# Optimization experiments

Measured on AMD Instinct MI355X. Metric: run time of the kernel, lower is better.

## Reference

```python
import jax, jax.numpy as jnp
import numpy as np

B, T, D, H = 4, 1024, 1024, 16
HD = D // H
EPS = 1e-5


def setup_inputs() -> dict:
    key = jax.random.key(0)
    ks = jax.random.split(key, 8)
    input_tensor = jax.random.normal(ks[0], (B, T, D), dtype=jnp.float32)
    # contiguous valid prefixes (realistic padding mask); True = valid
    lengths = jax.random.randint(ks[1], (B,), T // 2, T + 1)
    sequence_mask = jnp.arange(T)[None, :] < lengths[:, None]
    # online attention mask: causal (True = position allowed)
    attn_mask = jnp.tril(jnp.ones((T, T), dtype=bool))
    scale = 1.0 / np.sqrt(D)
    in_proj_w = jax.random.normal(ks[2], (3 * D, D), dtype=jnp.float32) * scale
    in_proj_b = jnp.zeros((3 * D,), dtype=jnp.float32)
    out_w = jax.random.normal(ks[3], (D, D), dtype=jnp.float32) * scale
    out_b = jnp.zeros((D,), dtype=jnp.float32)
    ln_gamma = jnp.ones((D,), dtype=jnp.float32)
    ln_beta = jnp.zeros((D,), dtype=jnp.float32)
    return {
        "input_tensor": input_tensor,
        "ln_gamma": ln_gamma,
        "ln_beta": ln_beta,
        "in_proj_w": in_proj_w,
        "in_proj_b": in_proj_b,
        "out_w": out_w,
        "out_b": out_b,
        "sequence_mask": sequence_mask,
        "attn_mask": attn_mask,
    }


def reference(input_tensor, ln_gamma, ln_beta, in_proj_w, in_proj_b, out_w, out_b,
              sequence_mask, attn_mask):
    # LayerNorm over last dim
    mu = jnp.mean(input_tensor, axis=-1, keepdims=True)
    var = jnp.mean(jnp.square(input_tensor - mu), axis=-1, keepdims=True)
    x = (input_tensor - mu) * jax.lax.rsqrt(var + EPS) * ln_gamma + ln_beta

    # shared QKV projection (torch MHA packed in_proj)
    qkv = x @ in_proj_w.T + in_proj_b  # [B,T,3D]
    q, k, v = jnp.split(qkv, 3, axis=-1)
    q = q.reshape(B, T, H, HD) * (1.0 / np.sqrt(HD))
    k = k.reshape(B, T, H, HD)
    v = v.reshape(B, T, H, HD)

    scores = jnp.einsum("bqhd,bkhd->bhqk", q, k)  # [B,H,T,T], shared

    keypad = sequence_mask[:, None, None, :]          # True = valid key
    online_ok = keypad & attn_mask[None, None, :, :]  # padding + attn mask
    neg_inf = jnp.float32(-jnp.inf)

    def attend(ok_mask):
        p = jax.nn.softmax(jnp.where(ok_mask, scores, neg_inf), axis=-1)
        o = jnp.einsum("bhqk,bkhd->bqhd", p, v).reshape(B, T, D)
        return o @ out_w.T + out_b

    out_online = attend(online_ok)   # key_padding + attn_mask
    out_offline = attend(keypad)     # key_padding only (full context)
    # training path: cat on dim 0 then view(2, B, T, D)
    return jnp.stack((out_online, out_offline), axis=0)
```

## Files before the change

kernel.cpp:

```cpp
#include <hip/hip_runtime.h>

#define B_ 4
#define T_ 1024
#define D_ 1024
#define H_ 16
#define HD_ 64

typedef unsigned short u16;
typedef __bf16 bf16x8 __attribute__((ext_vector_type(8)));
typedef float f32x4 __attribute__((ext_vector_type(4)));
typedef unsigned short u16x4 __attribute__((ext_vector_type(4)));

__device__ inline u16 f2b(float f) {
    union { float f; unsigned u; } v; v.f = f;
    unsigned r = v.u + 0x7fffu + ((v.u >> 16) & 1u);
    return (u16)(r >> 16);
}

__device__ inline f32x4 mfma16(bf16x8 a, bf16x8 b, f32x4 c) {
    return __builtin_amdgcn_mfma_f32_16x16x32_bf16(a, b, c, 0, 0, 0);
}

__global__ __launch_bounds__(256) void len_kernel(const unsigned char* __restrict__ m,
                                                  int* __restrict__ lens) {
    const int t = threadIdx.x;
    const int b = blockIdx.x;
    const int esz4 = (m[1] == 0);
    int c = 0;
    for (int i = t; i < T_; i += 256) {
        bool v = esz4 ? (((const int*)m)[b * T_ + i] != 0) : (m[b * T_ + i] != 0);
        c += v ? 1 : 0;
    }
#pragma unroll
    for (int off = 1; off < 64; off <<= 1) c += __shfl_xor(c, off);
    __shared__ int red[4];
    if ((t & 63) == 0) red[t >> 6] = c;
    __syncthreads();
    if (t == 0) lens[b] = red[0] + red[1] + red[2] + red[3];
}

__global__ __launch_bounds__(256) void cvt_bf16(const float* __restrict__ in,
                                                u16* __restrict__ out, int n4) {
    int i = blockIdx.x * 256 + threadIdx.x;
    int stride = gridDim.x * 256;
    for (; i < n4; i += stride) {
        float4 v = ((const float4*)in)[i];
        u16x4 o = { f2b(v.x), f2b(v.y), f2b(v.z), f2b(v.w) };
        ((u16x4*)out)[i] = o;
    }
}

__global__ __launch_bounds__(256) void ln_kernel(const float* __restrict__ x,
                                                 const float* __restrict__ g,
                                                 const float* __restrict__ be,
                                                 u16* __restrict__ y) {
    __shared__ float red[8];
    const int row = blockIdx.x;
    const int tid = threadIdx.x;
    const float* xr = x + (size_t)row * D_;
    float4 v = ((const float4*)xr)[tid];
    float s  = v.x + v.y + v.z + v.w;
    float ss = v.x*v.x + v.y*v.y + v.z*v.z + v.w*v.w;
#pragma unroll
    for (int off = 1; off < 64; off <<= 1) {
        s  += __shfl_xor(s, off);
        ss += __shfl_xor(ss, off);
    }
    const int w = tid >> 6;
    if ((tid & 63) == 0) { red[w*2] = s; red[w*2+1] = ss; }
    __syncthreads();
    s  = red[0] + red[2] + red[4] + red[6];
    ss = red[1] + red[3] + red[5] + red[7];
    const float mu = s * (1.f/1024.f);
    const float rs = rsqrtf(ss*(1.f/1024.f) - mu*mu + 1e-5f);
    float4 gv = ((const float4*)g)[tid];
    float4 bv = ((const float4*)be)[tid];
    u16x4 o = { f2b((v.x-mu)*rs*gv.x + bv.x),
                f2b((v.y-mu)*rs*gv.y + bv.y),
                f2b((v.z-mu)*rs*gv.z + bv.z),
                f2b((v.w-mu)*rs*gv.w + bv.w) };
    ((u16x4*)(y + (size_t)row * D_))[tid] = o;
}

template <int EPI>
__global__ __launch_bounds__(256) void gemm_bt(
    const u16* __restrict__ A, const u16* __restrict__ Bw,
    const float* __restrict__ bias, float* __restrict__ Cf,
    u16* __restrict__ Qb, u16* __restrict__ Kb, u16* __restrict__ Vt,
    int M, int N, int K) {
    __shared__ u16 As[128 * 64];
    __shared__ u16 Bs[128 * 64];
    const int tid = threadIdx.x;
    const int w = tid >> 6, l = tid & 63;
    const int l15 = l & 15, lg = l >> 4;
    const int m0 = blockIdx.y * 128, n0 = blockIdx.x * 128;
    const int wr = w >> 1, wc = w & 1;
    const int ldr = l >> 3;
    const int ldc = (l & 7) * 8;

    f32x4 acc[4][4];
#pragma unroll
    for (int m = 0; m < 4; m++)
#pragma unroll
        for (int n = 0; n < 4; n++) acc[m][n] = (f32x4){0.f, 0.f, 0.f, 0.f};

    for (int k0 = 0; k0 < K; k0 += 64) {
#pragma unroll
        for (int it = 0; it < 4; ++it) {
            const int c = it * 4 + w;
            const u16* ga = A  + (size_t)(m0 + c*8 + ldr) * K + (k0 + ldc);
            const u16* gb = Bw + (size_t)(n0 + c*8 + ldr) * K + (k0 + ldc);
            __builtin_amdgcn_global_load_lds(
                (const __attribute__((address_space(1))) unsigned int*)ga,
                (__attribute__((address_space(3))) unsigned int*)(As + c * 512), 16, 0, 0);
            __builtin_amdgcn_global_load_lds(
                (const __attribute__((address_space(1))) unsigned int*)gb,
                (__attribute__((address_space(3))) unsigned int*)(Bs + c * 512), 16, 0, 0);
        }
        __syncthreads();
#pragma unroll
        for (int kk = 0; kk < 64; kk += 32) {
            bf16x8 af[4], bfr[4];
#pragma unroll
            for (int m = 0; m < 4; m++)
                af[m] = *(const bf16x8*)&As[(wr*64 + m*16 + l15) * 64 + kk + lg*8];
#pragma unroll
            for (int n = 0; n < 4; n++)
                bfr[n] = *(const bf16x8*)&Bs[(wc*64 + n*16 + l15) * 64 + kk + lg*8];
#pragma unroll
            for (int m = 0; m < 4; m++)
#pragma unroll
                for (int n = 0; n < 4; n++)
                    acc[m][n] = mfma16(af[m], bfr[n], acc[m][n]);
        }
        __syncthreads();
    }

#pragma unroll
    for (int m = 0; m < 4; m++) {
#pragma unroll
        for (int n = 0; n < 4; n++) {
            const int col = n0 + wc*64 + n*16 + l15;
            const float bv = bias[col];
            if constexpr (EPI == 0) {
#pragma unroll
                for (int r = 0; r < 4; r++) {
                    const int row = m0 + wr*64 + m*16 + lg*4 + r;
                    Cf[(size_t)row * N + col] = acc[m][n][r] + bv;
                }
            } else {
                const int which = col >> 10;
                const int d = col & 1023;
                const int h = d >> 6, hd = d & 63;
#pragma unroll
                for (int r = 0; r < 4; r++) {
                    const int row = m0 + wr*64 + m*16 + lg*4 + r;
                    const int bb = row >> 10, t = row & 1023;
                    const float v = acc[m][n][r] + bv;
                    const size_t bh = (size_t)bb * H_ + h;
                    if (which == 0)      Qb[(bh * T_ + t) * HD_ + hd] = f2b(v * 0.125f);
                    else if (which == 1) Kb[(bh * T_ + t) * HD_ + hd] = f2b(v);
                    else                 Vt[(bh * HD_ + hd) * T_ + t] = f2b(v);
                }
            }
        }
    }
}

__global__ __launch_bounds__(256) void attn_kernel(
    const u16* __restrict__ Qb, const u16* __restrict__ Kb,
    const u16* __restrict__ Vt, const int* __restrict__ lens,
    u16* __restrict__ Ob) {
    __shared__ u16 Ks[2][64 * 64];
    __shared__ u16 Vs[2][64 * 64];
    __shared__ char Pl[4][2048];
    const int qt  = blockIdx.x;
    const int bh  = blockIdx.y;
    const int b = bh >> 4, h = bh & 15;
    const int tid = threadIdx.x, w = tid >> 6, l = tid & 63;
    const int l15 = l & 15, lg = l >> 4;
    const int len = lens[b];

    const u16* Qh = Qb + (size_t)bh * (T_ * HD_);
    const u16* Kh = Kb + (size_t)bh * (T_ * HD_);
    const u16* Vh = Vt + (size_t)bh * (HD_ * T_);

    const int q0 = qt * 64 + w * 16;
    const int qrow = q0 + l15;

    const bf16x8 qf0 = *(const bf16x8*)(Qh + (size_t)qrow * HD_ + lg * 8);
    const bf16x8 qf1 = *(const bf16x8*)(Qh + (size_t)qrow * HD_ + 32 + lg * 8);

    f32x4 acc0[4], acc1[4];
#pragma unroll
    for (int n = 0; n < 4; n++) {
        acc0[n] = (f32x4){0.f, 0.f, 0.f, 0.f};
        acc1[n] = (f32x4){0.f, 0.f, 0.f, 0.f};
    }
    float l0p = 0.f, l1p = 0.f;

    const int ntk = (len + 63) >> 6;

    char* Pw = &Pl[w][0];
    const int swz = (l15 & 7) << 4;
    const int rsw = l15 & 7;

    const int srow = l >> 3;
    const int scg  = (l & 7) ^ srow;

    const float C1 = 1.44269504f, C0 = -28.8539008f;

    auto stage = [&](int buf, int kt) {
        const int k0 = kt * 64;
#pragma unroll
        for (int c = 0; c < 2; ++c) {
            const int row = (w*2 + c)*8 + srow;
            const u16* gk = Kh + (size_t)(k0 + row) * HD_ + scg*8;
            const u16* gv = Vh + (size_t)row * T_ + k0 + scg*8;
            __builtin_amdgcn_global_load_lds(
                (const __attribute__((address_space(1))) unsigned int*)gk,
                (__attribute__((address_space(3))) unsigned int*)(&Ks[buf][(w*2+c)*512]), 16, 0, 0);
            __builtin_amdgcn_global_load_lds(
                (const __attribute__((address_space(1))) unsigned int*)gv,
                (__attribute__((address_space(3))) unsigned int*)(&Vs[buf][(w*2+c)*512]), 16, 0, 0);
        }
    };

    stage(0, 0);
    __syncthreads();

    int buf = 0;
    for (int kt = 0; kt < ntk; ++kt) {
        if (kt + 1 < ntk) stage(buf ^ 1, kt + 1);
        const int k0 = kt * 64;
        const u16* Kt = &Ks[buf][0];
        const u16* Vl = &Vs[buf][0];

        f32x4 s[4];
#pragma unroll
        for (int n = 0; n < 4; n++) {
            const u16* kr = Kt + (n*16 + l15) * 64;
            bf16x8 kf0 = *(const bf16x8*)&kr[((0 + lg) ^ rsw) * 8];
            bf16x8 kf1 = *(const bf16x8*)&kr[((4 + lg) ^ rsw) * 8];
            f32x4 z = (f32x4){0.f, 0.f, 0.f, 0.f};
            z = mfma16(kf0, qf0, z);
            z = mfma16(kf1, qf1, z);
            s[n] = z;
        }
        bf16x8 vf[4][2];
#pragma unroll
        for (int n = 0; n < 4; n++) {
            const u16* vr = Vl + (n*16 + l15) * 64;
            vf[n][0] = *(const bf16x8*)&vr[((0 + lg) ^ rsw) * 8];
            vf[n][1] = *(const bf16x8*)&vr[((4 + lg) ^ rsw) * 8];
        }
        float pn = 0.f;
#pragma unroll
        for (int n = 0; n < 4; n++) {
            const int kb = k0 + n*16 + lg*4;
#pragma unroll
            for (int r = 0; r < 4; r++) {
                const float e = (kb + r < len) ? exp2f(s[n][r]*C1 + C0) : 0.f;
                s[n][r] = e;
                pn += e;
            }
        }
        const bool diag = (kt == qt);
        if (diag) {
            l0p = l1p;
#pragma unroll
            for (int n = 0; n < 4; n++) acc0[n] = acc1[n];
        }
        l1p += pn;
#pragma unroll
        for (int n = 0; n < 4; n++) {
            u16x4 pk = { f2b(s[n][0]), f2b(s[n][1]), f2b(s[n][2]), f2b(s[n][3]) };
            *(u16x4*)(Pw + ((l15*128 + n*32 + lg*8) ^ swz)) = pk;
        }
#pragma unroll
        for (int kk = 0; kk < 2; ++kk) {
            bf16x8 pa = *(const bf16x8*)(Pw + ((l15*128 + kk*64 + lg*16) ^ swz));
#pragma unroll
            for (int n = 0; n < 4; n++)
                acc1[n] = mfma16(vf[n][kk], pa, acc1[n]);
        }
        if (diag) {
            float pn0 = 0.f;
#pragma unroll
            for (int n = 0; n < 4; n++) {
                const int kb = k0 + n*16 + lg*4;
#pragma unroll
                for (int r = 0; r < 4; r++) {
                    const float e = (kb + r <= qrow) ? s[n][r] : 0.f;
                    s[n][r] = e;
                    pn0 += e;
                }
            }
            l0p += pn0;
#pragma unroll
            for (int n = 0; n < 4; n++) {
                u16x4 pk = { f2b(s[n][0]), f2b(s[n][1]), f2b(s[n][2]), f2b(s[n][3]) };
                *(u16x4*)(Pw + ((l15*128 + n*32 + lg*8) ^ swz)) = pk;
            }
#pragma unroll
            for (int kk = 0; kk < 2; ++kk) {
                bf16x8 pa = *(const bf16x8*)(Pw + ((l15*128 + kk*64 + lg*16) ^ swz));
#pragma unroll
                for (int n = 0; n < 4; n++)
                    acc0[n] = mfma16(vf[n][kk], pa, acc0[n]);
            }
        }
        __syncthreads();
        buf ^= 1;
    }

    if (qt >= ntk) {
        l0p = l1p;
#pragma unroll
        for (int n = 0; n < 4; n++) acc0[n] = acc1[n];
    }

    float l0 = l0p + __shfl_xor(l0p, 16);
    l0 += __shfl_xor(l0, 32);
    float l1 = l1p + __shfl_xor(l1p, 16);
    l1 += __shfl_xor(l1, 32);

    const float inv0 = 1.f / l0;
    const float inv1 = 1.f / l1;
    u16* O0 = Ob + ((size_t)b * T_ + qrow) * D_ + h * HD_;
    u16* O1 = O0 + (size_t)B_ * T_ * D_;
#pragma unroll
    for (int n = 0; n < 4; n++) {
        u16x4 o0 = { f2b(acc0[n][0] * inv0), f2b(acc0[n][1] * inv0),
                     f2b(acc0[n][2] * inv0), f2b(acc0[n][3] * inv0) };
        u16x4 o1 = { f2b(acc1[n][0] * inv1), f2b(acc1[n][1] * inv1),
                     f2b(acc1[n][2] * inv1), f2b(acc1[n][3] * inv1) };
        *(u16x4*)(O0 + n*16 + lg*4) = o0;
        *(u16x4*)(O1 + n*16 + lg*4) = o1;
    }
}

extern "C" void kernel_launch(void* const* d_in, const int* in_sizes, int n_in,
                              void* d_out, int out_size, void* d_ws, size_t ws_size,
                              hipStream_t stream) {
    const float* x_in   = (const float*)d_in[0];
    const float* gamma  = (const float*)d_in[1];
    const float* beta   = (const float*)d_in[2];
    const float* wqkv_f = (const float*)d_in[3];
    const float* bqkv   = (const float*)d_in[4];
    const float* wout_f = (const float*)d_in[5];
    const float* bout   = (const float*)d_in[6];
    const unsigned char* smask = (const unsigned char*)d_in[7];
    float* out = (float*)d_out;

    char* ws = (char*)d_ws;
    u16* xb   = (u16*)(ws);
    u16* wqkv = (u16*)(ws + ((size_t)8  << 20));
    u16* wo   = (u16*)(ws + ((size_t)14 << 20));
    u16* Qb   = (u16*)(ws + ((size_t)16 << 20));
    u16* Kb   = (u16*)(ws + ((size_t)24 << 20));
    u16* Vt   = (u16*)(ws + ((size_t)32 << 20));
    u16* Ob   = (u16*)(ws + ((size_t)40 << 20));
    int* lens = (int*)(ws + ((size_t)56 << 20));

    len_kernel<<<dim3(B_), dim3(256), 0, stream>>>(smask, lens);
    cvt_bf16<<<dim3(1024), dim3(256), 0, stream>>>(wqkv_f, wqkv, (3 * D_ * D_) / 4);
    cvt_bf16<<<dim3(512),  dim3(256), 0, stream>>>(wout_f, wo, (D_ * D_) / 4);
    ln_kernel<<<dim3(B_ * T_), dim3(256), 0, stream>>>(x_in, gamma, beta, xb);
    gemm_bt<1><<<dim3(24, 32), dim3(256), 0, stream>>>(
        xb, wqkv, bqkv, nullptr, Qb, Kb, Vt, B_ * T_, 3 * D_, D_);
    attn_kernel<<<dim3(T_ / 64, B_ * H_), dim3(256), 0, stream>>>(Qb, Kb, Vt, lens, Ob);
    gemm_bt<0><<<dim3(8, 64), dim3(256), 0, stream>>>(
        Ob, wo, bout, out, nullptr, nullptr, nullptr, 2 * B_ * T_, D_, D_);
}
```

Baseline: 160.0 us.

## Double-buffer GEMM LDS tiles and XOR-swizzle layout to avoid bank conflicts

The bf16 GEMM now uses two LDS buffers so the global-to-LDS load of the next K tile is issued while MFMAs run on the current one, which takes load latency off the critical path. It also stores each 8-element column group at an XOR-swizzled position keyed by row and reads it back with the matching swizzle, to cut LDS bank conflicts on fragment reads. LDS use doubles to 64KB per block, which may limit occupancy. Correctness relies on the single barrier per iteration ordering the async loads, which is a possible hazard.

```diff
diff --git a/kernel.cpp b/kernel.cpp
--- a/kernel.cpp
+++ b/kernel.cpp
@@ -88,15 +88,16 @@
     const float* __restrict__ bias, float* __restrict__ Cf,
     u16* __restrict__ Qb, u16* __restrict__ Kb, u16* __restrict__ Vt,
     int M, int N, int K) {
-    __shared__ u16 As[128 * 64];
-    __shared__ u16 Bs[128 * 64];
+    __shared__ u16 As[2][128 * 64];
+    __shared__ u16 Bs[2][128 * 64];
     const int tid = threadIdx.x;
     const int w = tid >> 6, l = tid & 63;
     const int l15 = l & 15, lg = l >> 4;
     const int m0 = blockIdx.y * 128, n0 = blockIdx.x * 128;
     const int wr = w >> 1, wc = w & 1;
-    const int ldr = l >> 3;
-    const int ldc = (l & 7) * 8;
+    const int srow = l >> 3;
+    const int scg  = (l & 7) ^ srow;
+    const int swa  = l15 & 7;
 
     f32x4 acc[4][4];
 #pragma unroll
@@ -104,29 +105,40 @@
 #pragma unroll
         for (int n = 0; n < 4; n++) acc[m][n] = (f32x4){0.f, 0.f, 0.f, 0.f};
 
-    for (int k0 = 0; k0 < K; k0 += 64) {
+    const int KS = K >> 6;
+
+    auto stage = [&](int buf, int ks) {
+        const int k0 = ks * 64;
 #pragma unroll
         for (int it = 0; it < 4; ++it) {
             const int c = it * 4 + w;
-            const u16* ga = A  + (size_t)(m0 + c*8 + ldr) * K + (k0 + ldc);
-            const u16* gb = Bw + (size_t)(n0 + c*8 + ldr) * K + (k0 + ldc);
+            const int row = c * 8 + srow;
+            const u16* ga = A  + (size_t)(m0 + row) * K + (k0 + scg * 8);
+            const u16* gb = Bw + (size_t)(n0 + row) * K + (k0 + scg * 8);
             __builtin_amdgcn_global_load_lds(
                 (const __attribute__((address_space(1))) unsigned int*)ga,
-                (__attribute__((address_space(3))) unsigned int*)(As + c * 512), 16, 0, 0);
+                (__attribute__((address_space(3))) unsigned int*)(&As[buf][c * 512]), 16, 0, 0);
             __builtin_amdgcn_global_load_lds(
                 (const __attribute__((address_space(1))) unsigned int*)gb,
-                (__attribute__((address_space(3))) unsigned int*)(Bs + c * 512), 16, 0, 0);
-        }
-        __syncthreads();
-#pragma unroll
-        for (int kk = 0; kk < 64; kk += 32) {
+                (__attribute__((address_space(3))) unsigned int*)(&Bs[buf][c * 512]), 16, 0, 0);
+        }
+    };
+
+    stage(0, 0);
+    __syncthreads();
+
+    int buf = 0;
+    for (int ks = 0; ks < KS; ++ks) {
+        if (ks + 1 < KS) stage(buf ^ 1, ks + 1);
+#pragma unroll
+        for (int h = 0; h < 2; ++h) {
             bf16x8 af[4], bfr[4];
 #pragma unroll
             for (int m = 0; m < 4; m++)
-                af[m] = *(const bf16x8*)&As[(wr*64 + m*16 + l15) * 64 + kk + lg*8];
+                af[m] = *(const bf16x8*)&As[buf][(wr*64 + m*16 + l15) * 64 + ((h*4 + lg) ^ swa) * 8];
 #pragma unroll
             for (int n = 0; n < 4; n++)
-                bfr[n] = *(const bf16x8*)&Bs[(wc*64 + n*16 + l15) * 64 + kk + lg*8];
+                bfr[n] = *(const bf16x8*)&Bs[buf][(wc*64 + n*16 + l15) * 64 + ((h*4 + lg) ^ swa) * 8];
 #pragma unroll
             for (int m = 0; m < 4; m++)
 #pragma unroll
@@ -134,6 +146,7 @@
                     acc[m][n] = mfma16(af[m], bfr[n], acc[m][n]);
         }
         __syncthreads();
+        buf ^= 1;
     }
 
 #pragma unroll
```

After: 147.5 us. 7.8% less time.
